# Kernel tuning notes

Measured on AMD Instinct MI355X. Metric: run time of the kernel, lower is better.

The kernel has to match this reference:

```python
import jax, jax.numpy as jnp
import numpy as np

B, C, H, W = 16, 256, 56, 56
PH, PW = 7, 7            # partition (window) size
HEADS, DH = 8, 32        # n_heads = C // head_dim
P = PH * PW              # tokens per window = 49
GH, GW = H // PH, W // PW
G = GH * GW              # number of windows = 64
MLP = 4                  # mlp_ratio
EPS = 1e-5
SCALE = C ** (-0.5)      # note: torch code scales by feat_dim, not head_dim


def _rel_index(h, w):
    coords = np.stack(np.meshgrid(np.arange(h), np.arange(w), indexing='ij'))  # [2,h,w]
    cf = coords.reshape(2, -1)
    rel = cf[:, :, None] - cf[:, None, :]              # [2,P,P]
    rel = rel.transpose(1, 2, 0)
    rel[:, :, 0] += h - 1
    rel[:, :, 1] += w - 1
    rel[:, :, 0] *= 2 * w - 1
    return rel.sum(-1).astype(np.int32)                # [P,P]


def setup_inputs() -> dict:
    key = jax.random.key(0)
    ks = jax.random.split(key, 8)
    std = 0.02
    return {
        'x': jax.random.normal(ks[0], (B, C, H, W), jnp.float32),
        'ln1_g': jnp.ones((C,), jnp.float32),
        'ln1_b': jnp.zeros((C,), jnp.float32),
        'wqkv': jax.random.normal(ks[1], (C, 3 * C), jnp.float32) * std,
        'bqkv': jnp.zeros((3 * C,), jnp.float32),
        'wmerge': jax.random.normal(ks[2], (C, C), jnp.float32) * std,
        'bmerge': jnp.zeros((C,), jnp.float32),
        'bias_table': jax.random.normal(ks[3], ((2 * PH - 1) * (2 * PW - 1), HEADS), jnp.float32) * std,
        'ln2_g': jnp.ones((C,), jnp.float32),
        'ln2_b': jnp.zeros((C,), jnp.float32),
        'w1': jax.random.normal(ks[4], (C, MLP * C), jnp.float32) * std,
        'b1': jnp.zeros((MLP * C,), jnp.float32),
        'w2': jax.random.normal(ks[5], (MLP * C, C), jnp.float32) * std,
        'b2': jnp.zeros((C,), jnp.float32),
        'rel_idx': jnp.asarray(_rel_index(PH, PW)),
    }


def _layernorm(x, g, b):
    mu = jnp.mean(x, axis=-1, keepdims=True)
    var = jnp.var(x, axis=-1, keepdims=True)
    return (x - mu) * jax.lax.rsqrt(var + EPS) * g + b


def reference(x, ln1_g, ln1_b, wqkv, bqkv, wmerge, bmerge, bias_table,
              ln2_g, ln2_b, w1, b1, w2, b2, rel_idx):
    # --- window partition: [B,C,H,W] -> [B,G,P,C]
    xw = x.reshape(B, C, GH, PH, GW, PW).transpose(0, 2, 4, 3, 5, 1).reshape(B, G, P, C)

    # --- relative-position attention block
    y = _layernorm(xw, ln1_g, ln1_b)
    qkv = y @ wqkv + bqkv                               # [B,G,P,3C]
    q, k, v = jnp.split(qkv, 3, axis=-1)
    q = q.reshape(B, G, P, HEADS, DH)
    k = k.reshape(B, G, P, HEADS, DH) * SCALE
    v = v.reshape(B, G, P, HEADS, DH)
    scores = jnp.einsum('bgihd,bgjhd->bghij', q, k)     # [B,G,H,P,P]
    bias = bias_table[rel_idx].transpose(2, 0, 1)       # [H,P,P]
    attn = jax.nn.softmax(scores + bias[None, None], axis=-1)
    out = jnp.einsum('bghij,bgjhd->bgihd', attn, v).reshape(B, G, P, C)
    out = out @ wmerge + bmerge
    xw = xw + out

    # --- MLP block
    z = _layernorm(xw, ln2_g, ln2_b)
    z = jax.nn.gelu(z @ w1 + b1, approximate=False) @ w2 + b2
    xw = xw + z

    # --- window departition: [B,G,P,C] -> [B,C,H,W]
    xo = xw.reshape(B, GH, GW, PH, PW, C).transpose(0, 5, 1, 3, 2, 4).reshape(B, C, H, W)
    return xo
```

## Files before the change

kernel.cpp:

```cpp
#include <hip/hip_runtime.h>
#include <hip/hip_bf16.h>

#define B_      16
#define C_      256
#define H_      56
#define W_      56
#define HW_     3136
#define G_      64
#define P_      49
#define NTOK    50176
#define HEADS_  8
#define DH_     32
#define SCALE_  0.0625f
#define EPS_    1e-5f

typedef short bf16x8 __attribute__((ext_vector_type(8)));
typedef short bf16x4_t __attribute__((ext_vector_type(4)));
typedef float f32x4  __attribute__((ext_vector_type(4)));
using bf16 = __hip_bfloat16;

__device__ __forceinline__ void gload16(const void* g, void* l) {
  __builtin_amdgcn_global_load_lds((const __attribute__((address_space(1))) void*)g,
                                   (__attribute__((address_space(3))) void*)l, 16, 0, 0);
}
__device__ __forceinline__ float b2f(short s) {
  union { float f; unsigned u; } v; v.u = ((unsigned)(unsigned short)s) << 16; return v.f;
}
__device__ __forceinline__ short f2b(float f) {
  union { float f; unsigned u; } v; v.f = f;
  unsigned r = (v.u + 0x7FFFu + ((v.u >> 16) & 1u)) >> 16;
  return (short)r;
}

__global__ __launch_bounds__(256)
void prep_kernel(const float* __restrict__ wqkv, const float* __restrict__ wmerge,
                 const float* __restrict__ w1, const float* __restrict__ w2,
                 const float* __restrict__ btab, const int* __restrict__ relidx,
                 bf16* __restrict__ wqkvT, bf16* __restrict__ wmergeT,
                 bf16* __restrict__ w1T, bf16* __restrict__ w2T,
                 short* __restrict__ bt)
{
  int idx = blockIdx.x * 256 + threadIdx.x;
  if (idx < 196608) { int n = idx >> 8, k = idx & 255;
    wqkvT[idx] = __float2bfloat16(wqkv[k * 768 + n]); return; }
  idx -= 196608;
  if (idx < 65536) { int n = idx >> 8, k = idx & 255;
    wmergeT[idx] = __float2bfloat16(wmerge[k * 256 + n]); return; }
  idx -= 65536;
  if (idx < 262144) { int n = idx >> 8, k = idx & 255;
    w1T[idx] = __float2bfloat16(w1[k * 1024 + n]); return; }
  idx -= 262144;
  if (idx < 262144) { int n = idx >> 10, k = idx & 1023;
    w2T[idx] = __float2bfloat16(w2[k * 256 + n]); return; }
  idx -= 262144;
  if (idx < 32768) {
    int h = idx >> 12, rest = idx & 4095;
    int key = rest >> 6, col = rest & 63;
    int q = col >> 2, qni = col & 3;
    int query = qni * 16 + q;
    float v = 0.f;
    if (key < P_ && query < P_) v = btab[relidx[query * P_ + key] * HEADS_ + h];
    bt[idx] = f2b(v);
  }
}

__global__ __launch_bounds__(256)
void ingest_kernel(const float* __restrict__ x, const float* __restrict__ gam,
                   const float* __restrict__ bet, short* __restrict__ xtok,
                   short* __restrict__ y)
{
  __shared__ short Lt[56 * 260];
  const int h = blockIdx.x % 56, b = blockIdx.x / 56;
  const int tid = threadIdx.x;

  const float* xb = x + (size_t)b * 256 * HW_ + h * 56;
#pragma unroll
  for (int i = 0; i < 14; i++) {
    int idx = i * 256 + tid;
    int c = idx / 14, w4 = idx - c * 14;
    float4 v = *(const float4*)(xb + (size_t)c * HW_ + w4 * 4);
    Lt[(w4 * 4 + 0) * 260 + c] = f2b(v.x);
    Lt[(w4 * 4 + 1) * 260 + c] = f2b(v.y);
    Lt[(w4 * 4 + 2) * 260 + c] = f2b(v.z);
    Lt[(w4 * 4 + 3) * 260 + c] = f2b(v.w);
  }
  __syncthreads();

  const int lane = tid & 63, wv = tid >> 6;
  float4 gv = *(const float4*)(gam + lane * 4);
  float4 bv = *(const float4*)(bet + lane * 4);
  const int hdiv = h / 7, hmod = h - hdiv * 7;

  for (int t = 0; t < 14; t++) {
    int w = wv * 14 + t;
    bf16x4_t raw = *(const bf16x4_t*)&Lt[w * 260 + lane * 4];
    float f0 = b2f(raw[0]), f1 = b2f(raw[1]), f2 = b2f(raw[2]), f3 = b2f(raw[3]);
    float sum = f0 + f1 + f2 + f3;
    float sq  = f0*f0 + f1*f1 + f2*f2 + f3*f3;
#pragma unroll
    for (int off = 32; off > 0; off >>= 1) {
      sum += __shfl_xor(sum, off, 64);
      sq  += __shfl_xor(sq,  off, 64);
    }
    float mu = sum * (1.0f / 256.0f);
    float var = sq * (1.0f / 256.0f) - mu * mu;
    float rs = rsqrtf(var + EPS_);
    int wdiv = w / 7, wmod = w - wdiv * 7;
    int tok = b * HW_ + (hdiv * 8 + wdiv) * P_ + hmod * 7 + wmod;
    *(bf16x4_t*)(xtok + (size_t)tok * 256 + lane * 4) = raw;
    bf16x4_t o;
    o[0] = f2b((f0 - mu) * rs * gv.x + bv.x);
    o[1] = f2b((f1 - mu) * rs * gv.y + bv.y);
    o[2] = f2b((f2 - mu) * rs * gv.z + bv.z);
    o[3] = f2b((f3 - mu) * rs * gv.w + bv.w);
    *(bf16x4_t*)(y + (size_t)tok * 256 + lane * 4) = o;
  }
}

__global__ __launch_bounds__(256)
void ln2_kernel(const short* __restrict__ xw, const float* __restrict__ gam,
                const float* __restrict__ bet, short* __restrict__ z)
{
  const int t = blockIdx.x * 4 + (threadIdx.x >> 6);
  const int lane = threadIdx.x & 63;
  bf16x4_t raw = *(const bf16x4_t*)(xw + (size_t)t * 256 + lane * 4);
  float v[4];
#pragma unroll
  for (int j = 0; j < 4; j++) v[j] = b2f(raw[j]);
  float sum = v[0] + v[1] + v[2] + v[3];
  float sq  = v[0]*v[0] + v[1]*v[1] + v[2]*v[2] + v[3]*v[3];
#pragma unroll
  for (int off = 32; off > 0; off >>= 1) {
    sum += __shfl_xor(sum, off, 64);
    sq  += __shfl_xor(sq,  off, 64);
  }
  float mu = sum * (1.0f / 256.0f);
  float var = sq * (1.0f / 256.0f) - mu * mu;
  float rs = rsqrtf(var + EPS_);
  bf16x4_t o;
#pragma unroll
  for (int j = 0; j < 4; j++) {
    int c = lane * 4 + j;
    o[j] = f2b((v[j] - mu) * rs * gam[c] + bet[c]);
  }
  *(bf16x4_t*)(z + (size_t)t * 256 + lane * 4) = o;
}

__global__ __launch_bounds__(256)
void egress_kernel(const short* __restrict__ outtok, float* __restrict__ out)
{
  const int h = blockIdx.x % 56, b = blockIdx.x / 56;
  const int w = threadIdx.x & 63, cblk = threadIdx.x >> 6;
  const bool act = w < 56;
  const int wcl = act ? w : 55;
  const int tok = b * HW_ + ((h / 7) * 8 + wcl / 7) * P_ + (h % 7) * 7 + (wcl % 7);
  const short* src = outtok + (size_t)tok * 256 + cblk * 64;
  float* dst = out + ((size_t)b * 256 + cblk * 64) * HW_ + h * 56 + w;
#pragma unroll
  for (int j0 = 0; j0 < 64; j0 += 8) {
    bf16x8 r = *(const bf16x8*)(src + j0);
#pragma unroll
    for (int jj = 0; jj < 8; jj++)
      if (act) dst[(size_t)(j0 + jj) * HW_] = b2f(r[jj]);
  }
}

__global__ __launch_bounds__(64)
void attn_kernel(const short* __restrict__ qkv, const short* __restrict__ bt,
                 short* __restrict__ out)
{
  __shared__ short Pbuf[64 * 72];
  const int bid = blockIdx.x;
  const int h = bid & 7;
  const int t0 = (bid >> 3) * P_;
  const int lane = threadIdx.x;
  const int g = lane >> 4, q = lane & 15;

  const short* qb = qkv + (size_t)t0 * 768 + h * 32;

  bf16x8 vf[2][2];
#pragma unroll
  for (int kkt = 0; kkt < 2; kkt++)
#pragma unroll
    for (int n2 = 0; n2 < 2; n2++)
#pragma unroll
      for (int jj = 0; jj < 8; jj++) {
        int key = kkt * 32 + 8 * g + jj; key = key > 48 ? 48 : key;
        vf[kkt][n2][jj] = qb[(size_t)key * 768 + 512 + n2 * 16 + q];
      }

  bf16x8 kf[4], qf[4];
#pragma unroll
  for (int mi = 0; mi < 4; mi++) {
    int r_ = mi * 16 + q; r_ = r_ > 48 ? 48 : r_;
    kf[mi] = *(const bf16x8*)(qb + (size_t)r_ * 768 + 256 + 8 * g);
  }
#pragma unroll
  for (int ni = 0; ni < 4; ni++) {
    int r_ = ni * 16 + q; r_ = r_ > 48 ? 48 : r_;
    qf[ni] = *(const bf16x8*)(qb + (size_t)r_ * 768 + 8 * g);
  }

  f32x4 sacc[4][4] = {};
#pragma unroll
  for (int mi = 0; mi < 4; mi++)
#pragma unroll
    for (int ni = 0; ni < 4; ni++)
      sacc[mi][ni] = __builtin_amdgcn_mfma_f32_16x16x32_bf16(kf[mi], qf[ni], sacc[mi][ni], 0, 0, 0);

  float mx[4] = {-1e30f, -1e30f, -1e30f, -1e30f};
  const short* btb = bt + (size_t)(h * 64) * 64 + q * 4;
#pragma unroll
  for (int mi = 0; mi < 4; mi++)
#pragma unroll
    for (int r = 0; r < 4; r++) {
      int key = mi * 16 + 4 * g + r;
      bf16x4_t bv = *(const bf16x4_t*)(btb + key * 64);
      bool valid = key < P_;
#pragma unroll
      for (int ni = 0; ni < 4; ni++) {
        float s = valid ? fmaf(sacc[mi][ni][r], SCALE_, b2f(bv[ni])) : -1e30f;
        sacc[mi][ni][r] = s;
        mx[ni] = fmaxf(mx[ni], s);
      }
    }
#pragma unroll
  for (int ni = 0; ni < 4; ni++) {
    mx[ni] = fmaxf(mx[ni], __shfl_xor(mx[ni], 16, 64));
    mx[ni] = fmaxf(mx[ni], __shfl_xor(mx[ni], 32, 64));
  }
  float sm[4] = {0.f, 0.f, 0.f, 0.f};
#pragma unroll
  for (int mi = 0; mi < 4; mi++)
#pragma unroll
    for (int ni = 0; ni < 4; ni++)
#pragma unroll
      for (int r = 0; r < 4; r++) {
        float p = __expf(sacc[mi][ni][r] - mx[ni]);
        sacc[mi][ni][r] = p;
        sm[ni] += p;
      }
#pragma unroll
  for (int ni = 0; ni < 4; ni++) {
    sm[ni] += __shfl_xor(sm[ni], 16, 64);
    sm[ni] += __shfl_xor(sm[ni], 32, 64);
    sm[ni] = 1.0f / sm[ni];
  }
#pragma unroll
  for (int ni = 0; ni < 4; ni++)
#pragma unroll
    for (int mi = 0; mi < 4; mi++) {
      bf16x4_t pv;
#pragma unroll
      for (int r = 0; r < 4; r++) pv[r] = f2b(sacc[mi][ni][r] * sm[ni]);
      *(bf16x4_t*)&Pbuf[(ni * 16 + q) * 72 + mi * 16 + 4 * g] = pv;
    }
  __syncthreads();

  f32x4 oacc[4][2] = {};
#pragma unroll
  for (int kkt = 0; kkt < 2; kkt++) {
    bf16x8 paf[4];
#pragma unroll
    for (int qi = 0; qi < 4; qi++)
      paf[qi] = *(const bf16x8*)&Pbuf[(qi * 16 + q) * 72 + kkt * 32 + 8 * g];
#pragma unroll
    for (int qi = 0; qi < 4; qi++)
#pragma unroll
      for (int n2 = 0; n2 < 2; n2++)
        oacc[qi][n2] = __builtin_amdgcn_mfma_f32_16x16x32_bf16(paf[qi], vf[kkt][n2], oacc[qi][n2], 0, 0, 0);
  }

  short* ob = out + (size_t)t0 * 256 + h * 32;
#pragma unroll
  for (int qi = 0; qi < 4; qi++)
#pragma unroll
    for (int r = 0; r < 4; r++) {
      int query = qi * 16 + 4 * g + r;
      if (query < P_) {
#pragma unroll
        for (int n2 = 0; n2 < 2; n2++)
          ob[(size_t)query * 256 + n2 * 16 + q] = f2b(oacc[qi][n2][r]);
      }
    }
}

template<int EPI, int WN>
__global__ __launch_bounds__(128 * WN)
void gemm_kernel(const bf16* __restrict__ A, const bf16* __restrict__ Wt,
                 const float* __restrict__ bias, int N, int K,
                 bf16* __restrict__ outb, short* __restrict__ res_io)
{
  constexpr int THREADS = 128 * WN;
  constexpr int BN = 64 * WN;
  constexpr int RPP = THREADS / 4;
  constexpr int APASS = 128 / RPP;
  __shared__ __align__(16) bf16 As[128 * 32];
  __shared__ __align__(16) bf16 Bs[BN * 32];
  const int tid = threadIdx.x;
  const int lane = tid & 63;
  const int wave = tid >> 6;
  const int wr = wave / WN, wc = wave % WN;
  const int bm = blockIdx.y * 128, bn = blockIdx.x * BN;

  f32x4 acc[4][4] = {};

  const int trow = tid >> 2;
  const int tcol = ((tid & 3) ^ ((tid >> 3) & 3)) * 8;
  const bf16* aA[APASS];
  bf16* dA[APASS];
#pragma unroll
  for (int p = 0; p < APASS; p++) {
    aA[p] = A + (size_t)(bm + p * RPP + trow) * K + tcol;
    dA[p] = As + p * RPP * 32 + tid * 8;
  }
  const bf16* aB0 = Wt + (size_t)(bn + trow) * K + tcol;
  const bf16* aB1 = Wt + (size_t)(bn + RPP + trow) * K + tcol;
  bf16* dB0 = Bs + tid * 8;
  bf16* dB1 = Bs + RPP * 32 + tid * 8;

  const int kc_sw = ((lane >> 4) ^ ((lane >> 1) & 3)) * 8;
  const int rA = wr * 64 + (lane & 15);
  const int rB = wc * 64 + (lane & 15);

  for (int k0 = 0; k0 < K; k0 += 32) {
#pragma unroll
    for (int p = 0; p < APASS; p++) gload16(aA[p] + k0, dA[p]);
    gload16(aB0 + k0, dB0);
    gload16(aB1 + k0, dB1);
    __syncthreads();
    bf16x8 af[4], bfr[4];
#pragma unroll
    for (int i = 0; i < 4; i++) {
      af[i]  = *(const bf16x8*)(As + (rA + i * 16) * 32 + kc_sw);
      bfr[i] = *(const bf16x8*)(Bs + (rB + i * 16) * 32 + kc_sw);
    }
#pragma unroll
    for (int mi = 0; mi < 4; mi++)
#pragma unroll
      for (int ni = 0; ni < 4; ni++)
        acc[mi][ni] = __builtin_amdgcn_mfma_f32_16x16x32_bf16(af[mi], bfr[ni], acc[mi][ni], 0, 0, 0);
    __syncthreads();
  }

#pragma unroll
  for (int mi = 0; mi < 4; mi++) {
#pragma unroll
    for (int ni = 0; ni < 4; ni++) {
#pragma unroll
      for (int r = 0; r < 4; r++) {
        const int row = bm + wr * 64 + mi * 16 + (lane >> 4) * 4 + r;
        const int col = bn + wc * 64 + ni * 16 + (lane & 15);
        float v = acc[mi][ni][r] + bias[col];
        if (EPI == 0) {
          outb[(size_t)row * N + col] = __float2bfloat16(v);
        } else if (EPI == 1) {
          float gv = 0.5f * v * (1.0f + erff(v * 0.70710678118f));
          outb[(size_t)row * N + col] = __float2bfloat16(gv);
        } else {
          size_t o = (size_t)row * 256 + col;
          res_io[o] = f2b(v + b2f(res_io[o]));
        }
      }
    }
  }
}

extern "C" void kernel_launch(void* const* d_in, const int* in_sizes, int n_in,
                              void* d_out, int out_size, void* d_ws, size_t ws_size,
                              hipStream_t stream)
{
  const float* x      = (const float*)d_in[0];
  const float* ln1_g  = (const float*)d_in[1];
  const float* ln1_b  = (const float*)d_in[2];
  const float* wqkv   = (const float*)d_in[3];
  const float* bqkv   = (const float*)d_in[4];
  const float* wmerge = (const float*)d_in[5];
  const float* bmerge = (const float*)d_in[6];
  const float* btab   = (const float*)d_in[7];
  const float* ln2_g  = (const float*)d_in[8];
  const float* ln2_b  = (const float*)d_in[9];
  const float* w1     = (const float*)d_in[10];
  const float* b1     = (const float*)d_in[11];
  const float* w2     = (const float*)d_in[12];
  const float* b2     = (const float*)d_in[13];
  const int*   relidx = (const int*)d_in[14];
  float* out = (float*)d_out;

  char* ws = (char*)d_ws;
  bf16*  wqkvT   = (bf16*)(ws);
  bf16*  wmergeT = (bf16*)(ws + 393216);
  bf16*  w1T     = (bf16*)(ws + 524288);
  bf16*  w2T     = (bf16*)(ws + 1048576);
  short* battn   = (short*)(ws + 1572864);
  short* R1      = (short*)(ws + 1638400);
  short* R2      = (short*)(ws + 27328512);
  short* qkvc    = (short*)(ws + 53018624);
  short* attnc   = (short*)(ws + 91553792);
  short* hbuf    = (short*)(ws + 53018624);

  prep_kernel<<<3200, 256, 0, stream>>>(wqkv, wmerge, w1, w2, btab, relidx,
                                        wqkvT, wmergeT, w1T, w2T, battn);

  ingest_kernel<<<896, 256, 0, stream>>>(x, ln1_g, ln1_b, R1, R2);

  for (int c = 0; c < 2; ++c) {
    size_t r0 = (size_t)c * 25088;
    gemm_kernel<0, 4><<<dim3(3, 196), 512, 0, stream>>>(
        (const bf16*)(R2 + r0 * 256), wqkvT, bqkv, 768, 256, (bf16*)qkvc, nullptr);
    attn_kernel<<<4096, 64, 0, stream>>>(qkvc, battn, attnc);
    gemm_kernel<2, 2><<<dim3(2, 196), 256, 0, stream>>>(
        (const bf16*)attnc, wmergeT, bmerge, 256, 256, nullptr, R1 + r0 * 256);
  }

  ln2_kernel<<<NTOK / 4, 256, 0, stream>>>(R1, ln2_g, ln2_b, R2);

  for (int c = 0; c < 2; ++c) {
    size_t r0 = (size_t)c * 25088;
    gemm_kernel<1, 4><<<dim3(4, 196), 512, 0, stream>>>(
        (const bf16*)(R2 + r0 * 256), w1T, b1, 1024, 256, (bf16*)hbuf, nullptr);
    gemm_kernel<2, 2><<<dim3(2, 196), 256, 0, stream>>>(
        (const bf16*)hbuf, w2T, b2, 256, 1024, nullptr, R1 + r0 * 256);
  }

  egress_kernel<<<896, 256, 0, stream>>>(R1, out);
}
```

Baseline: 291.3 us.

## Restructure GEMMs: direct A-fragment loads, full-K weight staging, fused LN2, tanh GELU

```diff
diff --git a/kernel.cpp b/kernel.cpp
--- a/kernel.cpp
+++ b/kernel.cpp
@@ -19,10 +19,6 @@
 typedef float f32x4  __attribute__((ext_vector_type(4)));
 using bf16 = __hip_bfloat16;
 
-__device__ __forceinline__ void gload16(const void* g, void* l) {
-  __builtin_amdgcn_global_load_lds((const __attribute__((address_space(1))) void*)g,
-                                   (__attribute__((address_space(3))) void*)l, 16, 0, 0);
-}
 __device__ __forceinline__ float b2f(short s) {
   union { float f; unsigned u; } v; v.u = ((unsigned)(unsigned short)s) << 16; return v.f;
 }
@@ -118,35 +114,6 @@
 }
 
 __global__ __launch_bounds__(256)
-void ln2_kernel(const short* __restrict__ xw, const float* __restrict__ gam,
-                const float* __restrict__ bet, short* __restrict__ z)
-{
-  const int t = blockIdx.x * 4 + (threadIdx.x >> 6);
-  const int lane = threadIdx.x & 63;
-  bf16x4_t raw = *(const bf16x4_t*)(xw + (size_t)t * 256 + lane * 4);
-  float v[4];
-#pragma unroll
-  for (int j = 0; j < 4; j++) v[j] = b2f(raw[j]);
-  float sum = v[0] + v[1] + v[2] + v[3];
-  float sq  = v[0]*v[0] + v[1]*v[1] + v[2]*v[2] + v[3]*v[3];
-#pragma unroll
-  for (int off = 32; off > 0; off >>= 1) {
-    sum += __shfl_xor(sum, off, 64);
-    sq  += __shfl_xor(sq,  off, 64);
-  }
-  float mu = sum * (1.0f / 256.0f);
-  float var = sq * (1.0f / 256.0f) - mu * mu;
-  float rs = rsqrtf(var + EPS_);
-  bf16x4_t o;
-#pragma unroll
-  for (int j = 0; j < 4; j++) {
-    int c = lane * 4 + j;
-    o[j] = f2b((v[j] - mu) * rs * gam[c] + bet[c]);
-  }
-  *(bf16x4_t*)(z + (size_t)t * 256 + lane * 4) = o;
-}
-
-__global__ __launch_bounds__(256)
 void egress_kernel(const short* __restrict__ outtok, float* __restrict__ out)
 {
   const int h = blockIdx.x % 56, b = blockIdx.x / 56;
@@ -285,62 +252,120 @@
     }
 }
 
-template<int EPI, int WN>
-__global__ __launch_bounds__(128 * WN)
+template<int EPI, int BM, int BN, int KTOT, int NN, int MINW>
+__global__ __launch_bounds__((BM/64)*(BN/64)*64, MINW)
 void gemm_kernel(const bf16* __restrict__ A, const bf16* __restrict__ Wt,
-                 const float* __restrict__ bias, int N, int K,
-                 bf16* __restrict__ outb, short* __restrict__ res_io)
-{
-  constexpr int THREADS = 128 * WN;
-  constexpr int BN = 64 * WN;
-  constexpr int RPP = THREADS / 4;
-  constexpr int APASS = 128 / RPP;
-  __shared__ __align__(16) bf16 As[128 * 32];
-  __shared__ __align__(16) bf16 Bs[BN * 32];
+                 const float* __restrict__ bias,
+                 bf16* __restrict__ outb, short* __restrict__ res_io,
+                 short* __restrict__ z_out,
+                 const float* __restrict__ gam, const float* __restrict__ bet)
+{
+  constexpr int WR = BM / 64, WC = BN / 64;
+  constexpr int THREADS = WR * WC * 64;
+  constexpr int KC = (KTOT > 256 ? 256 : KTOT);
+  constexpr int LDW = KC + 8;
+  constexpr int CPR = KC / 8;
+  __shared__ __align__(16) short Ws[BN][LDW];
+  __shared__ float red1[(EPI == 3) ? BM : 1][(EPI == 3) ? WC : 1];
+  __shared__ float red2[(EPI == 3) ? BM : 1][(EPI == 3) ? WC : 1];
+
   const int tid = threadIdx.x;
   const int lane = tid & 63;
   const int wave = tid >> 6;
-  const int wr = wave / WN, wc = wave % WN;
-  const int bm = blockIdx.y * 128, bn = blockIdx.x * BN;
+  const int wr = wave / WC, wc = wave % WC;
+  const int bm = blockIdx.y * BM, bn = blockIdx.x * BN;
+  const int l15 = lane & 15, g = lane >> 4;
 
   f32x4 acc[4][4] = {};
 
-  const int trow = tid >> 2;
-  const int tcol = ((tid & 3) ^ ((tid >> 3) & 3)) * 8;
-  const bf16* aA[APASS];
-  bf16* dA[APASS];
-#pragma unroll
-  for (int p = 0; p < APASS; p++) {
-    aA[p] = A + (size_t)(bm + p * RPP + trow) * K + tcol;
-    dA[p] = As + p * RPP * 32 + tid * 8;
-  }
-  const bf16* aB0 = Wt + (size_t)(bn + trow) * K + tcol;
-  const bf16* aB1 = Wt + (size_t)(bn + RPP + trow) * K + tcol;
-  bf16* dB0 = Bs + tid * 8;
-  bf16* dB1 = Bs + RPP * 32 + tid * 8;
-
-  const int kc_sw = ((lane >> 4) ^ ((lane >> 1) & 3)) * 8;
-  const int rA = wr * 64 + (lane & 15);
-  const int rB = wc * 64 + (lane & 15);
-
-  for (int k0 = 0; k0 < K; k0 += 32) {
-#pragma unroll
-    for (int p = 0; p < APASS; p++) gload16(aA[p] + k0, dA[p]);
-    gload16(aB0 + k0, dB0);
-    gload16(aB1 + k0, dB1);
+  const bf16* Abase[4];
+  const int arow = bm + wr * 64 + l15;
+#pragma unroll
+  for (int mi = 0; mi < 4; mi++)
+    Abase[mi] = A + (size_t)(arow + mi * 16) * KTOT + g * 8;
+  const int brow = wc * 64 + l15;
+
+  for (int kc = 0; kc < KTOT; kc += KC) {
+#pragma unroll
+    for (int c = 0; c < BN * CPR / THREADS; c++) {
+      int idx = c * THREADS + tid;
+      int r = idx / CPR, cc = idx - r * CPR;
+      *(bf16x8*)&Ws[r][cc * 8] =
+          *(const bf16x8*)(Wt + (size_t)(bn + r) * KTOT + kc + cc * 8);
+    }
     __syncthreads();
-    bf16x8 af[4], bfr[4];
-#pragma unroll
-    for (int i = 0; i < 4; i++) {
-      af[i]  = *(const bf16x8*)(As + (rA + i * 16) * 32 + kc_sw);
-      bfr[i] = *(const bf16x8*)(Bs + (rB + i * 16) * 32 + kc_sw);
+#pragma unroll
+    for (int t = 0; t < KC / 32; t++) {
+      bf16x8 af[4], bfr[4];
+#pragma unroll
+      for (int mi = 0; mi < 4; mi++)
+        af[mi] = *(const bf16x8*)(Abase[mi] + kc + t * 32);
+#pragma unroll
+      for (int ni = 0; ni < 4; ni++)
+        bfr[ni] = *(const bf16x8*)&Ws[brow + ni * 16][g * 8 + t * 32];
+#pragma unroll
+      for (int mi = 0; mi < 4; mi++)
+#pragma unroll
+        for (int ni = 0; ni < 4; ni++)
+          acc[mi][ni] = __builtin_amdgcn_mfma_f32_16x16x32_bf16(af[mi], bfr[ni], acc[mi][ni], 0, 0, 0);
+    }
+    if (kc + KC < KTOT) __syncthreads();
+  }
+
+  const int orow0 = bm + wr * 64, ocol0 = bn + wc * 64;
+  float bv[4];
+#pragma unroll
+  for (int ni = 0; ni < 4; ni++) bv[ni] = bias[ocol0 + ni * 16 + l15];
+
+  if constexpr (EPI == 3) {
+    float gv[4], btv[4];
+#pragma unroll
+    for (int ni = 0; ni < 4; ni++) {
+      gv[ni]  = gam[ocol0 + ni * 16 + l15];
+      btv[ni] = bet[ocol0 + ni * 16 + l15];
     }
 #pragma unroll
     for (int mi = 0; mi < 4; mi++)
 #pragma unroll
-      for (int ni = 0; ni < 4; ni++)
-        acc[mi][ni] = __builtin_amdgcn_mfma_f32_16x16x32_bf16(af[mi], bfr[ni], acc[mi][ni], 0, 0, 0);
+      for (int r = 0; r < 4; r++) {
+        const int rowl = wr * 64 + mi * 16 + g * 4 + r;
+        float s1 = 0.f, s2 = 0.f;
+#pragma unroll
+        for (int ni = 0; ni < 4; ni++) {
+          const int col = ocol0 + ni * 16 + l15;
+          float v = acc[mi][ni][r] + bv[ni]
+                  + b2f(res_io[(size_t)(bm + rowl) * 256 + col]);
+          acc[mi][ni][r] = v;
+          s1 += v; s2 += v * v;
+        }
+#pragma unroll
+        for (int off = 1; off < 16; off <<= 1) {
+          s1 += __shfl_xor(s1, off, 64);
+          s2 += __shfl_xor(s2, off, 64);
+        }
+        if (l15 == 0) { red1[rowl][wc] = s1; red2[rowl][wc] = s2; }
+      }
     __syncthreads();
+#pragma unroll
+    for (int mi = 0; mi < 4; mi++)
+#pragma unroll
+      for (int r = 0; r < 4; r++) {
+        const int rowl = wr * 64 + mi * 16 + g * 4 + r;
+        float m1 = 0.f, m2 = 0.f;
+#pragma unroll
+        for (int j = 0; j < WC; j++) { m1 += red1[rowl][j]; m2 += red2[rowl][j]; }
+        float mu = m1 * (1.0f / 256.0f);
+        float var = m2 * (1.0f / 256.0f) - mu * mu;
+        float rs = rsqrtf(var + EPS_);
+#pragma unroll
+        for (int ni = 0; ni < 4; ni++) {
+          const int col = ocol0 + ni * 16 + l15;
+          float v = acc[mi][ni][r];
+          res_io[(size_t)(bm + rowl) * 256 + col] = f2b(v);
+          z_out [(size_t)(bm + rowl) * 256 + col] = f2b((v - mu) * rs * gv[ni] + btv[ni]);
+        }
+      }
+    return;
   }
 
 #pragma unroll
@@ -349,14 +374,16 @@
     for (int ni = 0; ni < 4; ni++) {
 #pragma unroll
       for (int r = 0; r < 4; r++) {
-        const int row = bm + wr * 64 + mi * 16 + (lane >> 4) * 4 + r;
-        const int col = bn + wc * 64 + ni * 16 + (lane & 15);
-        float v = acc[mi][ni][r] + bias[col];
+        const int row = orow0 + mi * 16 + g * 4 + r;
+        const int col = ocol0 + ni * 16 + l15;
+        float v = acc[mi][ni][r] + bv[ni];
         if (EPI == 0) {
-          outb[(size_t)row * N + col] = __float2bfloat16(v);
+          outb[(size_t)row * NN + col] = __float2bfloat16(v);
         } else if (EPI == 1) {
-          float gv = 0.5f * v * (1.0f + erff(v * 0.70710678118f));
-          outb[(size_t)row * N + col] = __float2bfloat16(gv);
+          float u = 0.7978845608f * v * (1.0f + 0.044715f * v * v);
+          float e = __expf(2.0f * u);
+          float th = 1.0f - 2.0f / (e + 1.0f);
+          outb[(size_t)row * NN + col] = __float2bfloat16(0.5f * v * (1.0f + th));
         } else {
           size_t o = (size_t)row * 256 + col;
           res_io[o] = f2b(v + b2f(res_io[o]));
@@ -406,21 +433,23 @@
 
   for (int c = 0; c < 2; ++c) {
     size_t r0 = (size_t)c * 25088;
-    gemm_kernel<0, 4><<<dim3(3, 196), 512, 0, stream>>>(
-        (const bf16*)(R2 + r0 * 256), wqkvT, bqkv, 768, 256, (bf16*)qkvc, nullptr);
+    gemm_kernel<0, 256, 128, 256, 768, 4><<<dim3(6, 98), 512, 0, stream>>>(
+        (const bf16*)(R2 + r0 * 256), wqkvT, bqkv, (bf16*)qkvc,
+        nullptr, nullptr, nullptr, nullptr);
     attn_kernel<<<4096, 64, 0, stream>>>(qkvc, battn, attnc);
-    gemm_kernel<2, 2><<<dim3(2, 196), 256, 0, stream>>>(
-        (const bf16*)attnc, wmergeT, bmerge, 256, 256, nullptr, R1 + r0 * 256);
-  }
-
-  ln2_kernel<<<NTOK / 4, 256, 0, stream>>>(R1, ln2_g, ln2_b, R2);
+    gemm_kernel<3, 128, 256, 256, 256, 2><<<dim3(1, 196), 512, 0, stream>>>(
+        (const bf16*)attnc, wmergeT, bmerge, nullptr,
+        R1 + r0 * 256, R2 + r0 * 256, ln2_g, ln2_b);
+  }
 
   for (int c = 0; c < 2; ++c) {
     size_t r0 = (size_t)c * 25088;
-    gemm_kernel<1, 4><<<dim3(4, 196), 512, 0, stream>>>(
-        (const bf16*)(R2 + r0 * 256), w1T, b1, 1024, 256, (bf16*)hbuf, nullptr);
-    gemm_kernel<2, 2><<<dim3(2, 196), 256, 0, stream>>>(
-        (const bf16*)hbuf, w2T, b2, 256, 1024, nullptr, R1 + r0 * 256);
+    gemm_kernel<1, 256, 128, 256, 1024, 4><<<dim3(8, 98), 512, 0, stream>>>(
+        (const bf16*)(R2 + r0 * 256), w1T, b1, (bf16*)hbuf,
+        nullptr, nullptr, nullptr, nullptr);
+    gemm_kernel<2, 128, 128, 1024, 256, 2><<<dim3(2, 196), 256, 0, stream>>>(
+        (const bf16*)hbuf, w2T, b2, nullptr,
+        R1 + r0 * 256, nullptr, nullptr, nullptr);
   }
 
   egress_kernel<<<896, 256, 0, stream>>>(R1, out);
```

Result: slower. 381.9 us (+31.1%).
